# Kernel tuning notes

Hardware: AMD Instinct MI355X
Metric: run time of the kernel (lower is better)

Reference implementation:

```python
import jax, jax.numpy as jnp
import numpy as np

H, W, C = 384, 384, 200
HIDE, CNN_OUT, NCLS = 128, 64, 16
N = H * W
E = 1179648
EPS = 1e-5  # torch BatchNorm eps


def _bn(x, g, b, axes):
    # training-mode batch norm (biased variance), matches torch BN in train mode
    m = x.mean(axes, keepdims=True)
    v = x.var(axes, keepdims=True)
    return (x - m) * jax.lax.rsqrt(v + EPS) * g + b


def _gcn(x, w, bias, src, dst, n):
    # PyG GCNConv: add self loops, symmetric D^-1/2 (A+I) D^-1/2 normalization
    h = x @ w  # [N, out]
    loop = jnp.arange(n, dtype=src.dtype)
    s = jnp.concatenate([src, loop])
    d = jnp.concatenate([dst, loop])
    deg = jax.ops.segment_sum(jnp.ones(s.shape, x.dtype), d, num_segments=n)
    dinv = jnp.where(deg > 0, jax.lax.rsqrt(jnp.maximum(deg, 1.0)) * (deg > 0), 0.0)
    norm = dinv[s] * dinv[d]  # [E+N]
    out = jax.ops.segment_sum(h[s] * norm[:, None], d, num_segments=n)
    return out + bias


def _gnn_layer(x, bn_g, bn_b, w, b, src, dst):
    # F.normalize (row L2) -> BN1d -> GCNConv -> LeakyReLU (dropout off in eval)
    nrm = jnp.linalg.norm(x, axis=1, keepdims=True)
    x = x / jnp.maximum(nrm, 1e-12)
    x = _bn(x, bn_g, bn_b, (0,))
    return jax.nn.leaky_relu(_gcn(x, w, b, src, dst, x.shape[0]))


def setup_inputs() -> dict:
    key = jax.random.key(0)
    ks = jax.random.split(key, 16)
    p = {}
    p["x"] = jax.random.normal(ks[0], (H, W, C), jnp.float32)
    p["edge_index"] = jax.random.randint(ks[1], (2, E), 0, N, jnp.int32)
    # CNN_denoise: BN(C) -> 1x1 conv C->128 -> BN(128) -> 1x1 conv 128->128
    p["dn_bn1_g"] = jnp.ones((C,), jnp.float32); p["dn_bn1_b"] = jnp.zeros((C,), jnp.float32)
    p["dn_w1"] = jax.random.normal(ks[2], (C, HIDE), jnp.float32) * 0.05
    p["dn_b1"] = jnp.zeros((HIDE,), jnp.float32)
    p["dn_bn2_g"] = jnp.ones((HIDE,), jnp.float32); p["dn_bn2_b"] = jnp.zeros((HIDE,), jnp.float32)
    p["dn_w2"] = jax.random.normal(ks[3], (HIDE, HIDE), jnp.float32) * 0.05
    p["dn_b2"] = jnp.zeros((HIDE,), jnp.float32)
    # CNNCONV(128,64,k=5): BN(128) -> point 1x1 128->64 (no bias) -> depthwise 5x5 (bias)
    p["cnn_bn_g"] = jnp.ones((HIDE,), jnp.float32); p["cnn_bn_b"] = jnp.zeros((HIDE,), jnp.float32)
    p["cnn_pw"] = jax.random.normal(ks[4], (HIDE, CNN_OUT), jnp.float32) * 0.05
    p["cnn_dw"] = jax.random.normal(ks[5], (CNN_OUT, 1, 5, 5), jnp.float32) * 0.05
    p["cnn_db"] = jnp.zeros((CNN_OUT,), jnp.float32)
    # GCN branch: GNN(128,128), GNN(128,128), GNN(128,64)
    dims = [(HIDE, HIDE), (HIDE, HIDE), (HIDE, CNN_OUT)]
    for i, (di, do) in enumerate(dims, 1):
        p[f"g{i}_bn_g"] = jnp.ones((di,), jnp.float32)
        p[f"g{i}_bn_b"] = jnp.zeros((di,), jnp.float32)
        p[f"g{i}_w"] = jax.random.normal(ks[5 + i], (di, do), jnp.float32) * 0.05
        p[f"g{i}_b"] = jnp.zeros((do,), jnp.float32)
    p["lin_w"] = jax.random.normal(ks[9], (HIDE, NCLS), jnp.float32) * 0.05
    p["lin_b"] = jnp.zeros((NCLS,), jnp.float32)
    return p


def reference(x, edge_index,
              dn_bn1_g, dn_bn1_b, dn_w1, dn_b1, dn_bn2_g, dn_bn2_b, dn_w2, dn_b2,
              cnn_bn_g, cnn_bn_b, cnn_pw, cnn_dw, cnn_db,
              g1_bn_g, g1_bn_b, g1_w, g1_b,
              g2_bn_g, g2_bn_b, g2_w, g2_b,
              g3_bn_g, g3_bn_b, g3_w, g3_b,
              lin_w, lin_b):
    src, dst = edge_index[0], edge_index[1]
    # CNN_denoise (channel-last; 1x1 convs are matmuls)
    h = _bn(x, dn_bn1_g, dn_bn1_b, (0, 1))
    h = jax.nn.leaky_relu(h @ dn_w1 + dn_b1)
    h = _bn(h, dn_bn2_g, dn_bn2_b, (0, 1))
    clean = jax.nn.leaky_relu(h @ dn_w2 + dn_b2)       # [H,W,128]
    flat = clean.reshape(N, HIDE)
    # CNN branch: BN -> 1x1 -> LeakyReLU -> depthwise 5x5 -> LeakyReLU
    c = _bn(clean, cnn_bn_g, cnn_bn_b, (0, 1))
    c = jax.nn.leaky_relu(c @ cnn_pw)                  # [H,W,64]
    cn = c.transpose(2, 0, 1)[None]                    # [1,64,H,W]
    cn = jax.lax.conv_general_dilated(
        cn, cnn_dw, (1, 1), 'SAME', feature_group_count=CNN_OUT,
        dimension_numbers=('NCHW', 'OIHW', 'NCHW'))
    cn = jax.nn.leaky_relu(cn[0].transpose(1, 2, 0) + cnn_db)
    cnn_res = cn.reshape(N, CNN_OUT)
    # GCN branch (3 layers)
    g = _gnn_layer(flat, g1_bn_g, g1_bn_b, g1_w, g1_b, src, dst)
    g = _gnn_layer(g, g2_bn_g, g2_bn_b, g2_w, g2_b, src, dst)
    g = _gnn_layer(g, g3_bn_g, g3_bn_b, g3_w, g3_b, src, dst)
    y = jnp.concatenate([g, cnn_res], axis=-1) @ lin_w + lin_b
    return jax.nn.softmax(y, axis=-1)
```

## Files before the change

kernel.cpp:

```cpp
#include <hip/hip_runtime.h>
#include <stddef.h>

#define HH 384
#define WW 384
#define CC 200
#define NN 147456
#define EE 1179648
#define HIDE 128
#define COUT 64
#define NCLS 16
#define BN_EPS 1e-5f

#define SREP 16
#define SLOTF (512 * SREP)
#define DBINS 64

#define NBKT 72
#define NPBK 288
#define EPB  4096

using u16 = unsigned short;
typedef __attribute__((ext_vector_type(8))) short short8;
typedef __attribute__((ext_vector_type(4))) float float4v;

__device__ __forceinline__ float b2f(u16 u) {
    union { unsigned int i; float f; } v; v.i = ((unsigned int)u) << 16; return v.f;
}
__device__ __forceinline__ u16 f2b(float f) {
    union { float f; unsigned int i; } v; v.f = f;
    unsigned int x = v.i;
    unsigned int r = (x + 0x7fffu + ((x >> 16) & 1u)) >> 16;
    return (u16)r;
}
__device__ __forceinline__ float lrelu(float v) { return v > 0.f ? v : 0.01f * v; }

__global__ void sniff(const u16* __restrict__ x, int* __restrict__ flag) {
    __shared__ int cntS;
    if (threadIdx.x == 0) cntS = 0;
    __syncthreads();
    int c = 0;
    for (int i = 0; i < 8; i++) {
        u16 h = x[threadIdx.x * 8 + i];
        int hb = (h >> 8) & 0x7F;
        if (hb >= 0x3C && hb <= 0x41) c++;
    }
    atomicAdd(&cntS, c);
    __syncthreads();
    if (threadIdx.x == 0) *flag = (cntS < 1536) ? 1 : 0;
}

#define NPAR 27
struct PConv { const void* src[NPAR]; int n[NPAR]; int off[NPAR]; };

__global__ void convert_params(PConv pc, const int* __restrict__ flag,
                               u16* __restrict__ dst) {
    int b = blockIdx.x;
    int n = pc.n[b];
    const void* s = pc.src[b];
    u16* d = dst + pc.off[b];
    int isf = *flag;
    if (isf) {
        const float* sf = (const float*)s;
        for (int i = threadIdx.x; i < n; i += 256) d[i] = f2b(sf[i]);
    } else {
        const u16* sh = (const u16*)s;
        for (int i = threadIdx.x; i < n; i += 256) d[i] = sh[i];
    }
}

__global__ __launch_bounds__(256) void stats200(const void* __restrict__ X,
                                                const int* __restrict__ flag,
                                                float* __restrict__ arena) {
    __shared__ __align__(16) u16 s[128 * 200];
    int t = threadIdx.x;
    int r0 = blockIdx.x * 128;
    if (*flag) {
        const float* Xf = (const float*)X;
        for (int i = t; i < 128 * 25; i += 256) {
            int r = i / 25, kc = i - r * 25;
            const float* p = Xf + (size_t)(r0 + r) * CC + kc * 8;
            float4v a = *(const float4v*)p;
            float4v b = *(const float4v*)(p + 4);
            short8 v;
            #pragma unroll
            for (int j = 0; j < 4; j++) { v[j] = (short)f2b(a[j]); v[4 + j] = (short)f2b(b[j]); }
            *(short8*)&s[r * 200 + kc * 8] = v;
        }
    } else {
        const u16* Xh = (const u16*)X;
        for (int i = t; i < 128 * 25; i += 256) {
            int r = i / 25, kc = i - r * 25;
            *(short8*)&s[r * 200 + kc * 8] =
                *(const short8*)(Xh + (size_t)(r0 + r) * CC + kc * 8);
        }
    }
    __syncthreads();
    if (t < CC) {
        float sum = 0.f, sq = 0.f;
        for (int r = 0; r < 128; r++) {
            float v = b2f(s[r * 200 + t]);
            sum += v; sq += v * v;
        }
        float* rep = arena + (blockIdx.x & (SREP - 1)) * 512;
        atomicAdd(&rep[t], sum);
        atomicAdd(&rep[256 + t], sq);
    }
}

template<int K, int KPAD, int O>
__global__ __launch_bounds__(256) void fold_bn(
        const float* __restrict__ arena, float invN,
        const u16* __restrict__ bng, const u16* __restrict__ bnb,
        const u16* __restrict__ Wsrc, const u16* __restrict__ extrab,
        u16* __restrict__ WT, float* __restrict__ cb) {
    __shared__ float aS[KPAD], sS[KPAD];
    int t = threadIdx.x;
    if (t < KPAD) {
        float a = 0.f, sh = 0.f;
        if (t < K) {
            float sum = 0.f, sq = 0.f;
            #pragma unroll
            for (int r = 0; r < SREP; r++) {
                sum += arena[r * 512 + t];
                sq  += arena[r * 512 + 256 + t];
            }
            float m = sum * invN;
            float var = fmaxf(sq * invN - m * m, 0.f);
            a = b2f(bng[t]) * rsqrtf(var + BN_EPS);
            sh = b2f(bnb[t]) - m * a;
        }
        aS[t] = a; sS[t] = sh;
    }
    __syncthreads();
    int g = t >> 6, l = t & 63;
    int o = blockIdx.x * 4 + g;
    if (o < O) {
        float c = 0.f;
        #pragma unroll
        for (int k = l; k < KPAD; k += 64) {
            float w = (k < K) ? b2f(Wsrc[k * O + o]) : 0.f;
            c += sS[k] * w;
            WT[o * KPAD + k] = f2b(aS[k] * w);
        }
        #pragma unroll
        for (int s = 32; s >= 1; s >>= 1) c += __shfl_down(c, s);
        if (l == 0) cb[o] = c + (extrab ? b2f(extrab[o]) : 0.f);
    }
}

template<int KT, int KSRC, int O, bool LEAKY, bool SCALE, int STATS, bool DUAL>
__global__ __launch_bounds__(256) void gemm_mfma(
        const void* __restrict__ Ap, const u16* __restrict__ WT,
        const float* __restrict__ cb, const float* __restrict__ s1,
        const float* __restrict__ s2, const int* __restrict__ f32p,
        u16* __restrict__ out, float* __restrict__ stA,
        float* __restrict__ stB, float* __restrict__ invn,
        u16* __restrict__ out2) {
    constexpr int KPAD = KT * 32;
    constexpr int LDA = KPAD + 8;
    constexpr int CHR = KPAD / 8;
    constexpr int CHD = KSRC / 8;
    constexpr int NCT = O / 16;
    constexpr int CPW = NCT / 4;
    __shared__ __align__(16) u16 As[64 * LDA];
    __shared__ float rS[4][64];
    __shared__ float invS[64];
    __shared__ float sS1[64], sS2[64];
    int tid = threadIdx.x;
    int row0 = blockIdx.x * 64;

    int isf = f32p ? *f32p : 0;
    if (isf) {
        const float* A = (const float*)Ap;
        for (int i = tid; i < 64 * CHR; i += 256) {
            int r = i / CHR, kc = i - r * CHR;
            short8 v = {0, 0, 0, 0, 0, 0, 0, 0};
            if (kc < CHD) {
                const float* p = A + (size_t)(row0 + r) * KSRC + kc * 8;
                float4v a = *(const float4v*)p;
                float4v b = *(const float4v*)(p + 4);
                #pragma unroll
                for (int j = 0; j < 4; j++) { v[j] = (short)f2b(a[j]); v[4 + j] = (short)f2b(b[j]); }
            }
            *(short8*)&As[r * LDA + kc * 8] = v;
        }
    } else {
        const u16* A = (const u16*)Ap;
        for (int i = tid; i < 64 * CHR; i += 256) {
            int r = i / CHR, kc = i - r * CHR;
            short8 v = {0, 0, 0, 0, 0, 0, 0, 0};
            if (kc < CHD)
                v = *(const short8*)(A + (size_t)(row0 + r) * KSRC + kc * 8);
            *(short8*)&As[r * LDA + kc * 8] = v;
        }
    }
    if (SCALE && tid < 64) { sS1[tid] = s1[row0 + tid]; sS2[tid] = s2[row0 + tid]; }
    __syncthreads();

    int w = tid >> 6, lane = tid & 63, m = lane & 15, q = lane >> 4;
    float4v acc[4][CPW];
    #pragma unroll
    for (int mf = 0; mf < 4; mf++)
        #pragma unroll
        for (int cp = 0; cp < CPW; cp++)
            acc[mf][cp] = (float4v){0.f, 0.f, 0.f, 0.f};

    const u16* Abp = &As[m * LDA + q * 8];
    const u16* Bbp = WT + (size_t)((w * CPW) * 16 + m) * KPAD + q * 8;

    #pragma unroll
    for (int kt = 0; kt < KT; kt++) {
        short8 af[4];
        #pragma unroll
        for (int mf = 0; mf < 4; mf++)
            af[mf] = *(const short8*)(Abp + mf * 16 * LDA + kt * 32);
        #pragma unroll
        for (int cp = 0; cp < CPW; cp++) {
            short8 bf = *(const short8*)(Bbp + (size_t)cp * 16 * KPAD + kt * 32);
            #pragma unroll
            for (int mf = 0; mf < 4; mf++)
                acc[mf][cp] = __builtin_amdgcn_mfma_f32_16x16x32_bf16(
                    af[mf], bf, acc[mf][cp], 0, 0, 0);
        }
    }

    float rp[4][4] = {};
    #pragma unroll
    for (int cp = 0; cp < CPW; cp++) {
        int ct = w * CPW + cp;
        int col = ct * 16 + m;
        float cbv = cb[col];
        #pragma unroll
        for (int mf = 0; mf < 4; mf++) {
            #pragma unroll
            for (int r = 0; r < 4; r++) {
                int rl = mf * 16 + q * 4 + r;
                float x = acc[mf][cp][r];
                if constexpr (DUAL) {
                    if (ct < 8) {
                        x = (x * sS1[rl] + cbv) * sS2[rl];
                        out[(size_t)(row0 + rl) * 128 + col] = f2b(x);
                    } else {
                        x = lrelu(x + cbv);
                        out2[(size_t)(row0 + rl) * 64 + (col - 128)] = f2b(x);
                    }
                } else {
                    if constexpr (SCALE) x = (x * sS1[rl] + cbv) * sS2[rl];
                    else                 x += cbv;
                    if constexpr (LEAKY) x = lrelu(x);
                    out[(size_t)(row0 + rl) * O + col] = f2b(x);
                }
                acc[mf][cp][r] = x;
                if constexpr (STATS == 2) rp[mf][r] += x * x;
            }
        }
    }

    if constexpr (STATS == 2) {
        #pragma unroll
        for (int mf = 0; mf < 4; mf++) {
            #pragma unroll
            for (int r = 0; r < 4; r++) {
                float v = rp[mf][r];
                v += __shfl_xor(v, 1); v += __shfl_xor(v, 2);
                v += __shfl_xor(v, 4); v += __shfl_xor(v, 8);
                if (m == 0) rS[w][mf * 16 + q * 4 + r] = v;
            }
        }
        __syncthreads();
        if (tid < 64) {
            float ss = rS[0][tid] + rS[1][tid] + rS[2][tid] + rS[3][tid];
            float inv = 1.0f / fmaxf(sqrtf(ss), 1e-12f);
            invS[tid] = inv;
            invn[row0 + tid] = inv;
        }
        __syncthreads();
    }

    if constexpr (STATS >= 1) {
        float* stAr = stA + (blockIdx.x & (SREP - 1)) * 512;
        float* stBr = (STATS == 2) ? stB + (blockIdx.x & (SREP - 1)) * 512 : nullptr;
        #pragma unroll
        for (int cp = 0; cp < CPW; cp++) {
            int col = (w * CPW + cp) * 16 + m;
            float cs = 0.f, cq = 0.f, ns = 0.f, nq = 0.f;
            #pragma unroll
            for (int mf = 0; mf < 4; mf++) {
                #pragma unroll
                for (int r = 0; r < 4; r++) {
                    float x = acc[mf][cp][r];
                    cs += x; cq += x * x;
                    if constexpr (STATS == 2) {
                        float nv = x * invS[mf * 16 + q * 4 + r];
                        ns += nv; nq += nv * nv;
                    }
                }
            }
            cs += __shfl_xor(cs, 16); cs += __shfl_xor(cs, 32);
            cq += __shfl_xor(cq, 16); cq += __shfl_xor(cq, 32);
            if constexpr (STATS == 2) {
                ns += __shfl_xor(ns, 16); ns += __shfl_xor(ns, 32);
                nq += __shfl_xor(nq, 16); nq += __shfl_xor(nq, 32);
            }
            if (q == 0) {
                atomicAdd(&stAr[col], cs);
                atomicAdd(&stAr[256 + col], cq);
                if constexpr (STATS == 2) {
                    atomicAdd(&stBr[col], ns);
                    atomicAdd(&stBr[256 + col], nq);
                }
            }
        }
    }
}

__global__ __launch_bounds__(256) void count_bkt(const int* __restrict__ edst,
                                                 int* __restrict__ counts) {
    __shared__ int h[NBKT];
    int t = threadIdx.x, blk = blockIdx.x;
    if (t < NBKT) h[t] = 0;
    __syncthreads();
    int base = blk * EPB;
    for (int i = t; i < EPB; i += 256) {
        unsigned d = (unsigned)edst[base + i];
        if (d < (unsigned)NN) atomicAdd(&h[d >> 11], 1);
    }
    __syncthreads();
    if (t < NBKT) counts[t * NPBK + blk] = h[t];
}

__global__ void scan_bkt(int* __restrict__ counts, int* __restrict__ bbase) {
    __shared__ int bs[NBKT], bb[NBKT];
    int t = threadIdx.x;
    if (t < NBKT) {
        int s = 0;
        for (int i = 0; i < NPBK; i++) s += counts[t * NPBK + i];
        bs[t] = s;
    }
    __syncthreads();
    if (t == 0) {
        int a = 0;
        for (int b = 0; b < NBKT; b++) { bb[b] = a; bbase[b] = a; a += bs[b]; }
        bbase[NBKT] = a;
    }
    __syncthreads();
    if (t < NBKT) {
        int run = bb[t];
        for (int i = 0; i < NPBK; i++) {
            int c = counts[t * NPBK + i];
            counts[t * NPBK + i] = run;
            run += c;
        }
    }
}

__global__ __launch_bounds__(256) void part_bkt(const int* __restrict__ esrc,
                                                const int* __restrict__ edst,
                                                const int* __restrict__ counts,
                                                int2* __restrict__ bpair) {
    __shared__ int cur[NBKT];
    int t = threadIdx.x, blk = blockIdx.x;
    if (t < NBKT) cur[t] = counts[t * NPBK + blk];
    __syncthreads();
    int base = blk * EPB;
    for (int i = t; i < EPB; i += 256) {
        unsigned d = (unsigned)edst[base + i];
        if (d < (unsigned)NN) {
            int pos = atomicAdd(&cur[d >> 11], 1);
            int2 p; p.x = esrc[base + i]; p.y = (int)d;
            bpair[pos] = p;
        }
    }
}

__global__ __launch_bounds__(256) void csr_build(const int2* __restrict__ bpair,
                                                 const int* __restrict__ bbase,
                                                 int* __restrict__ offv,
                                                 int* __restrict__ csr) {
    __shared__ int cntL[2048];
    __shared__ int exL[2048];
    __shared__ int tsum[256];
    int b = blockIdx.x, t = threadIdx.x;
    int e0 = bbase[b], e1 = bbase[b + 1];
    int n0 = b << 11;
    for (int i = t; i < 2048; i += 256) cntL[i] = 0;
    __syncthreads();
    for (int k = e0 + t; k < e1; k += 256) {
        int2 p = bpair[k];
        atomicAdd(&cntL[p.y & 2047], 1);
    }
    __syncthreads();
    int s = 0;
    #pragma unroll
    for (int j = 0; j < 8; j++) s += cntL[t * 8 + j];
    tsum[t] = s;
    __syncthreads();
    for (int o = 1; o < 256; o <<= 1) {
        int x = (t >= o) ? tsum[t - o] : 0;
        __syncthreads();
        tsum[t] += x;
        __syncthreads();
    }
    int run = tsum[t] - s;
    #pragma unroll
    for (int j = 0; j < 8; j++) { int c = cntL[t * 8 + j]; exL[t * 8 + j] = run; run += c; }
    __syncthreads();
    for (int i = t; i < 2048; i += 256) offv[n0 + i] = e0 + exL[i];
    if (b == NBKT - 1 && t == 0) offv[NN] = e1;
    for (int i = t; i < 2048; i += 256) cntL[i] = 0;
    __syncthreads();
    for (int k = e0 + t; k < e1; k += 256) {
        int2 p = bpair[k];
        int l = p.y & 2047;
        int pos = e0 + exL[l] + atomicAdd(&cntL[l], 1);
        csr[pos] = p.x;
    }
}

__global__ void mkdinv2(const int* __restrict__ offv, float* __restrict__ dinv) {
    int i = blockIdx.x * 256 + threadIdx.x;
    dinv[i] = rsqrtf((float)(offv[i + 1] - offv[i]) + 1.0f);
}

__global__ void deg_hist(const int* __restrict__ offv, int* __restrict__ dbin) {
    __shared__ int h[DBINS];
    int t = threadIdx.x;
    if (t < DBINS) h[t] = 0;
    __syncthreads();
    int i = blockIdx.x * 256 + t;
    int dg = offv[i + 1] - offv[i];
    if (dg < 0) dg = 0; if (dg > DBINS - 1) dg = DBINS - 1;
    atomicAdd(&h[dg], 1);
    __syncthreads();
    if (t < DBINS) atomicAdd(&dbin[t], h[t]);
}
__global__ void deg_scan(const int* __restrict__ dbin, int* __restrict__ dbase) {
    if (threadIdx.x == 0) {
        int a = 0;
        for (int b = DBINS - 1; b >= 0; b--) { dbase[b] = a; a += dbin[b]; }
    }
}
__global__ void deg_scatter(const int* __restrict__ offv, int* __restrict__ dbase,
                            int* __restrict__ perm) {
    __shared__ int h[DBINS], base[DBINS];
    int t = threadIdx.x;
    if (t < DBINS) h[t] = 0;
    __syncthreads();
    int i = blockIdx.x * 256 + t;
    int dg = offv[i + 1] - offv[i];
    if (dg < 0) dg = 0; if (dg > DBINS - 1) dg = DBINS - 1;
    atomicAdd(&h[dg], 1);
    __syncthreads();
    if (t < DBINS) { base[t] = atomicAdd(&dbase[t], h[t]); h[t] = 0; }
    __syncthreads();
    int lp = atomicAdd(&h[dg], 1);
    perm[base[dg] + lp] = i;
}

template<int O, int STATS, int GRP>
__global__ __launch_bounds__(256) void aggregate(
        const u16* __restrict__ h2, const int* __restrict__ offv,
        const int* __restrict__ csr, const float* __restrict__ dinv,
        const u16* __restrict__ gb, u16* __restrict__ outp,
        float* __restrict__ stA, float* __restrict__ invn,
        const int* __restrict__ perm) {
    constexpr int CH = O / 8;
    constexpr int NPB = 256 / CH;
    __shared__ float colS[O], colQ[O];
    int t = threadIdx.x;
    if (STATS && t < O) { colS[t] = 0.f; colQ[t] = 0.f; }
    int local = t / CH, c = t % CH;
    size_t cof = (size_t)c * 8;
    const u16* hb = h2 + cof;
    short8 gv = *(const short8*)(gb + cof);
    float sreg[8] = {0.f, 0.f, 0.f, 0.f, 0.f, 0.f, 0.f, 0.f};
    float qreg[8] = {0.f, 0.f, 0.f, 0.f, 0.f, 0.f, 0.f, 0.f};

    #pragma unroll
    for (int g = 0; g < GRP; g++) {
        int pos = blockIdx.x * (NPB * GRP) + g * NPB + local;
        int d = perm[pos];
        float acc[8];
        short8 selfv = *(const short8*)(hb + (size_t)d * O);
        #pragma unroll
        for (int j = 0; j < 8; j++) acc[j] = b2f((u16)selfv[j]);
        int e0 = offv[d], e1 = offv[d + 1];
        if (e0 < 0) e0 = 0;
        if (e1 > EE) e1 = EE;
        int k = e0;
        for (; k + 8 <= e1; k += 8) {
            unsigned i0 = (unsigned)csr[k],     i1 = (unsigned)csr[k + 1];
            unsigned i2 = (unsigned)csr[k + 2], i3 = (unsigned)csr[k + 3];
            unsigned i4 = (unsigned)csr[k + 4], i5 = (unsigned)csr[k + 5];
            unsigned i6 = (unsigned)csr[k + 6], i7 = (unsigned)csr[k + 7];
            short8 v0 = *(const short8*)(hb + (size_t)i0 * O);
            short8 v1 = *(const short8*)(hb + (size_t)i1 * O);
            short8 v2 = *(const short8*)(hb + (size_t)i2 * O);
            short8 v3 = *(const short8*)(hb + (size_t)i3 * O);
            short8 v4 = *(const short8*)(hb + (size_t)i4 * O);
            short8 v5 = *(const short8*)(hb + (size_t)i5 * O);
            short8 v6 = *(const short8*)(hb + (size_t)i6 * O);
            short8 v7 = *(const short8*)(hb + (size_t)i7 * O);
            #pragma unroll
            for (int j = 0; j < 8; j++)
                acc[j] += ((b2f((u16)v0[j]) + b2f((u16)v1[j])) +
                           (b2f((u16)v2[j]) + b2f((u16)v3[j]))) +
                          ((b2f((u16)v4[j]) + b2f((u16)v5[j])) +
                           (b2f((u16)v6[j]) + b2f((u16)v7[j])));
        }
        if (k + 4 <= e1) {
            unsigned i0 = (unsigned)csr[k],     i1 = (unsigned)csr[k + 1];
            unsigned i2 = (unsigned)csr[k + 2], i3 = (unsigned)csr[k + 3];
            short8 v0 = *(const short8*)(hb + (size_t)i0 * O);
            short8 v1 = *(const short8*)(hb + (size_t)i1 * O);
            short8 v2 = *(const short8*)(hb + (size_t)i2 * O);
            short8 v3 = *(const short8*)(hb + (size_t)i3 * O);
            #pragma unroll
            for (int j = 0; j < 8; j++)
                acc[j] += (b2f((u16)v0[j]) + b2f((u16)v1[j])) +
                          (b2f((u16)v2[j]) + b2f((u16)v3[j]));
            k += 4;
        }
        if (k + 2 <= e1) {
            unsigned i0 = (unsigned)csr[k], i1 = (unsigned)csr[k + 1];
            short8 v0 = *(const short8*)(hb + (size_t)i0 * O);
            short8 v1 = *(const short8*)(hb + (size_t)i1 * O);
            #pragma unroll
            for (int j = 0; j < 8; j++)
                acc[j] += b2f((u16)v0[j]) + b2f((u16)v1[j]);
            k += 2;
        }
        if (k < e1) {
            unsigned i0 = (unsigned)csr[k];
            short8 v0 = *(const short8*)(hb + (size_t)i0 * O);
            #pragma unroll
            for (int j = 0; j < 8; j++) acc[j] += b2f((u16)v0[j]);
        }
        float dd = dinv[d];
        float outv[8];
        short8 res;
        #pragma unroll
        for (int j = 0; j < 8; j++) {
            outv[j] = lrelu(dd * acc[j] + b2f((u16)gv[j]));
            res[j] = (short)f2b(outv[j]);
        }
        *(short8*)(outp + (size_t)d * O + cof) = res;

        if constexpr (STATS) {
            float ss = 0.f;
            #pragma unroll
            for (int j = 0; j < 8; j++) ss += outv[j] * outv[j];
            ss += __shfl_xor(ss, 1); ss += __shfl_xor(ss, 2);
            ss += __shfl_xor(ss, 4); ss += __shfl_xor(ss, 8);
            float inv = 1.0f / fmaxf(sqrtf(ss), 1e-12f);
            if (c == 0) invn[d] = inv;
            #pragma unroll
            for (int j = 0; j < 8; j++) {
                float nv = outv[j] * inv;
                sreg[j] += nv; qreg[j] += nv * nv;
            }
        }
    }

    if constexpr (STATS) {
        __syncthreads();
        #pragma unroll
        for (int j = 0; j < 8; j++) {
            float s = sreg[j];
            s += __shfl_xor(s, 16); s += __shfl_xor(s, 32);
            float qq = qreg[j];
            qq += __shfl_xor(qq, 16); qq += __shfl_xor(qq, 32);
            if ((t & 63) < 16) {
                atomicAdd(&colS[c * 8 + j], s);
                atomicAdd(&colQ[c * 8 + j], qq);
            }
        }
        __syncthreads();
        if (t < O) {
            float* rep = stA + (blockIdx.x & (SREP - 1)) * 512;
            atomicAdd(&rep[t], colS[t]);
            atomicAdd(&rep[256 + t], colQ[t]);
        }
    }
}

__global__ __launch_bounds__(256) void final_fused(
        const u16* __restrict__ g3, const u16* __restrict__ cpre,
        const u16* __restrict__ dwW, const u16* __restrict__ db,
        const u16* __restrict__ lw, const u16* __restrict__ lb,
        const int* __restrict__ flag, void* __restrict__ outp) {
    __shared__ __align__(16) u16 tile[400 * 72];
    __shared__ __align__(16) u16 wT[25 * 64];
    __shared__ __align__(16) u16 wL[2048];
    __shared__ float bDW[64];
    __shared__ float bL[16];
    int t = threadIdx.x;
    int tx = blockIdx.x % 24, ty = blockIdx.x / 24;
    int x0 = tx * 16 - 2, y0 = ty * 16 - 2;
    for (int i = t; i < 1600; i += 256) {
        int f = i / 25, tap = i - f * 25;
        wT[tap * 64 + f] = dwW[i];
    }
    for (int i = t; i < 2048; i += 256) wL[i] = lw[i];
    if (t < 64) bDW[t] = b2f(db[t]);
    if (t < 16) bL[t] = b2f(lb[t]);
    for (int u = t; u < 3200; u += 256) {
        int pix = u >> 3, c8 = u & 7;
        int gy = y0 + pix / 20, gx = x0 + pix % 20;
        short8 v = {0, 0, 0, 0, 0, 0, 0, 0};
        if (gy >= 0 && gy < HH && gx >= 0 && gx < WW)
            v = *(const short8*)(cpre + ((size_t)(gy * WW + gx)) * 64 + c8 * 8);
        *(short8*)&tile[pix * 72 + c8 * 8] = v;
    }
    __syncthreads();

    int px = t & 15, py = t >> 4;
    int node = (ty * 16 + py) * WW + tx * 16 + px;
    float y[16];
    #pragma unroll
    for (int o = 0; o < 16; o++) y[o] = bL[o];

    const u16* g3p = g3 + (size_t)node * 64;
    for (int c8 = 0; c8 < 8; c8++) {
        short8 gvv = *(const short8*)(g3p + c8 * 8);
        #pragma unroll
        for (int j = 0; j < 8; j++) {
            float g = b2f((u16)gvv[j]);
            const short8 w0 = *(const short8*)&wL[(c8 * 8 + j) * 16];
            const short8 w1 = *(const short8*)&wL[(c8 * 8 + j) * 16 + 8];
            #pragma unroll
            for (int o = 0; o < 8; o++) {
                y[o]     += g * b2f((u16)w0[o]);
                y[o + 8] += g * b2f((u16)w1[o]);
            }
        }
    }
    for (int c8 = 0; c8 < 8; c8++) {
        float acc[8] = {0.f, 0.f, 0.f, 0.f, 0.f, 0.f, 0.f, 0.f};
        #pragma unroll
        for (int dy = 0; dy < 5; dy++) {
            int rbase = ((py + dy) * 20 + px) * 72 + c8 * 8;
            #pragma unroll
            for (int dx = 0; dx < 5; dx++) {
                short8 v  = *(const short8*)&tile[rbase + dx * 72];
                short8 wv = *(const short8*)&wT[(dy * 5 + dx) * 64 + c8 * 8];
                #pragma unroll
                for (int j = 0; j < 8; j++)
                    acc[j] += b2f((u16)v[j]) * b2f((u16)wv[j]);
            }
        }
        #pragma unroll
        for (int j = 0; j < 8; j++) {
            float cv = lrelu(acc[j] + bDW[c8 * 8 + j]);
            int f = 64 + c8 * 8 + j;
            const short8 w0 = *(const short8*)&wL[f * 16];
            const short8 w1 = *(const short8*)&wL[f * 16 + 8];
            #pragma unroll
            for (int o = 0; o < 8; o++) {
                y[o]     += cv * b2f((u16)w0[o]);
                y[o + 8] += cv * b2f((u16)w1[o]);
            }
        }
    }
    float mx = y[0];
    #pragma unroll
    for (int o = 1; o < 16; o++) mx = fmaxf(mx, y[o]);
    float sum = 0.f;
    #pragma unroll
    for (int o = 0; o < 16; o++) { y[o] = __expf(y[o] - mx); sum += y[o]; }
    float inv = 1.0f / fmaxf(sum, 1e-30f);
    if (*flag) {
        float* of = (float*)outp;
        #pragma unroll
        for (int o = 0; o < 16; o++) of[(size_t)node * 16 + o] = y[o] * inv;
    } else {
        u16* oh = (u16*)outp;
        #pragma unroll
        for (int o = 0; o < 16; o++) oh[(size_t)node * 16 + o] = f2b(y[o] * inv);
    }
}

extern "C" void kernel_launch(void* const* d_in, const int* in_sizes, int n_in,
                              void* d_out, int out_size, void* d_ws, size_t ws_size,
                              hipStream_t stream) {
    const void* X   = d_in[0];
    const int* EIDX = (const int*)d_in[1];
    const int* esrc = EIDX;
    const int* edst = EIDX + EE;

    char* ws = (char*)d_ws;
    size_t off = 0;
    auto alloc = [&](size_t sz) -> char* {
        size_t szr = (sz + 255) & ~(size_t)255;
        char* p;
        if (off + szr <= ws_size) { p = ws + off; off += szr; }
        else { p = ws; }
        return p;
    };

    int*   dflag   = (int*)alloc(256);
    static const int pidx[NPAR] = {2,3,4,5,6,7,8,9,10,11,12,13,14,
                                   15,16,17,18,19,20,21,22,23,24,25,26,27,28};
    static const int pn[NPAR]   = {200,200,25600,128,128,128,16384,128,
                                   128,128,8192,1600,64,
                                   128,128,16384,128,
                                   128,128,16384,128,
                                   128,128,8192,64,
                                   2048,16};
    u16* parena = (u16*)alloc(100352 * 2);
    PConv pc;
    {
        int po = 0;
        for (int i = 0; i < NPAR; i++) {
            pc.src[i] = d_in[pidx[i]];
            pc.n[i] = pn[i];
            pc.off[i] = po;
            po += (pn[i] + 15) & ~15;
        }
    }
    const u16* DN1G = parena + pc.off[0];
    const u16* DN1B = parena + pc.off[1];
    const u16* DNW1 = parena + pc.off[2];
    const u16* DNB1 = parena + pc.off[3];
    const u16* DN2G = parena + pc.off[4];
    const u16* DN2B = parena + pc.off[5];
    const u16* DNW2 = parena + pc.off[6];
    const u16* DNB2 = parena + pc.off[7];
    const u16* CBNG = parena + pc.off[8];
    const u16* CBNB = parena + pc.off[9];
    const u16* CPW  = parena + pc.off[10];
    const u16* CDW  = parena + pc.off[11];
    const u16* CDB  = parena + pc.off[12];
    const u16* G1G  = parena + pc.off[13];
    const u16* G1B  = parena + pc.off[14];
    const u16* G1W  = parena + pc.off[15];
    const u16* G1BI = parena + pc.off[16];
    const u16* G2G  = parena + pc.off[17];
    const u16* G2B  = parena + pc.off[18];
    const u16* G2W  = parena + pc.off[19];
    const u16* G2BI = parena + pc.off[20];
    const u16* G3G  = parena + pc.off[21];
    const u16* G3B  = parena + pc.off[22];
    const u16* G3W  = parena + pc.off[23];
    const u16* G3BI = parena + pc.off[24];
    const u16* LINW = parena + pc.off[25];
    const u16* LINB = parena + pc.off[26];

    float* arena   = (float*)alloc((size_t)6 * SLOTF * 4);
    int*   dbin    = (int*)alloc(DBINS * 4);
    int*   counts  = (int*)alloc((size_t)NBKT * NPBK * 4);
    int*   bbase   = (int*)alloc((NBKT + 1) * 4);
    int2*  bpair   = (int2*)alloc((size_t)EE * 8);
    int*   offv    = (int*)alloc((size_t)(NN + 1) * 4);
    int*   dbase   = (int*)alloc(DBINS * 4);
    int*   perm    = (int*)alloc((size_t)NN * 4);
    float* dinvp   = (float*)alloc((size_t)NN * 4);
    float* invnorm = (float*)alloc((size_t)NN * 4);
    u16*   W1T     = (u16*)alloc(128 * 224 * 2);
    u16*   W2T     = (u16*)alloc(128 * 128 * 2);
    u16*   WgT     = (u16*)alloc(192 * 128 * 2);
    float* cb1     = (float*)alloc(128 * 4);
    float* cb2     = (float*)alloc(128 * 4);
    float* cbg     = (float*)alloc(192 * 4);
    int*   csr     = (int*)alloc((size_t)EE * 4);
    u16*   cbuf    = (u16*)alloc((size_t)NN * 64 * 2);
    u16*   big1    = (u16*)alloc((size_t)NN * 128 * 2);
    u16*   big2    = (u16*)alloc((size_t)NN * 128 * 2);

    const float invN = 1.0f / (float)NN;
    size_t zsz = (size_t)((char*)dbin + 256 - (char*)arena);
    size_t zcap = ((char*)arena >= ws && (size_t)((char*)arena - ws) < ws_size)
                      ? ws_size - (size_t)((char*)arena - ws) : 0;
    if (zsz > zcap) zsz = zcap;
    hipMemsetAsync(arena, 0, zsz, stream);

    sniff<<<1, 256, 0, stream>>>((const u16*)X, dflag);
    convert_params<<<NPAR, 256, 0, stream>>>(pc, dflag, parena);

    count_bkt<<<NPBK, 256, 0, stream>>>(edst, counts);
    scan_bkt<<<1, 128, 0, stream>>>(counts, bbase);
    part_bkt<<<NPBK, 256, 0, stream>>>(esrc, edst, counts, bpair);
    csr_build<<<NBKT, 256, 0, stream>>>(bpair, bbase, offv, csr);
    mkdinv2<<<NN / 256, 256, 0, stream>>>(offv, dinvp);
    deg_hist<<<NN / 256, 256, 0, stream>>>(offv, dbin);
    deg_scan<<<1, 64, 0, stream>>>(dbin, dbase);
    deg_scatter<<<NN / 256, 256, 0, stream>>>(offv, dbase, perm);

    stats200<<<1152, 256, 0, stream>>>(X, dflag, arena + 0 * SLOTF);
    fold_bn<200, 224, 128><<<32, 256, 0, stream>>>(arena + 0 * SLOTF, invN, DN1G, DN1B, DNW1, DNB1, W1T, cb1);
    gemm_mfma<7, 200, 128, true, false, 1, false><<<NN / 64, 256, 0, stream>>>(
        X, W1T, cb1, nullptr, nullptr, dflag, big1, arena + 1 * SLOTF, nullptr, nullptr, nullptr);
    fold_bn<128, 128, 128><<<32, 256, 0, stream>>>(arena + 1 * SLOTF, invN, DN2G, DN2B, DNW2, DNB2, W2T, cb2);
    gemm_mfma<4, 128, 128, true, false, 2, false><<<NN / 64, 256, 0, stream>>>(
        big1, W2T, cb2, nullptr, nullptr, nullptr, big2, arena + 2 * SLOTF, arena + 3 * SLOTF, invnorm, nullptr);

    fold_bn<128, 128, 128><<<32, 256, 0, stream>>>(arena + 3 * SLOTF, invN, G1G, G1B, G1W, nullptr, WgT, cbg);
    fold_bn<128, 128, 64><<<16, 256, 0, stream>>>(arena + 2 * SLOTF, invN, CBNG, CBNB, CPW, nullptr,
                                                  WgT + 128 * 128, cbg + 128);
    gemm_mfma<4, 128, 192, false, true, 0, true><<<NN / 64, 256, 0, stream>>>(
        big2, WgT, cbg, invnorm, dinvp, nullptr, big1, nullptr, nullptr, nullptr, cbuf);
    aggregate<128, 1, 4><<<NN / 64, 256, 0, stream>>>(
        big1, offv, csr, dinvp, G1BI, big2, arena + 4 * SLOTF, invnorm, perm);

    fold_bn<128, 128, 128><<<32, 256, 0, stream>>>(arena + 4 * SLOTF, invN, G2G, G2B, G2W, nullptr, WgT, cbg);
    gemm_mfma<4, 128, 128, false, true, 0, false><<<NN / 64, 256, 0, stream>>>(
        big2, WgT, cbg, invnorm, dinvp, nullptr, big1, nullptr, nullptr, nullptr, nullptr);
    aggregate<128, 1, 4><<<NN / 64, 256, 0, stream>>>(
        big1, offv, csr, dinvp, G2BI, big2, arena + 5 * SLOTF, invnorm, perm);

    fold_bn<128, 128, 64><<<16, 256, 0, stream>>>(arena + 5 * SLOTF, invN, G3G, G3B, G3W, nullptr, WgT, cbg);
    gemm_mfma<4, 128, 64, false, true, 0, false><<<NN / 64, 256, 0, stream>>>(
        big2, WgT, cbg, invnorm, dinvp, nullptr, big1, nullptr, nullptr, nullptr, nullptr);
    aggregate<64, 0, 1><<<NN / 32, 256, 0, stream>>>(
        big1, offv, csr, dinvp, G3BI, big2, nullptr, nullptr, perm);

    final_fused<<<576, 256, 0, stream>>>(big2, cbuf, CDW, CDB, LINW, LINB, dflag, d_out);

    (void)in_sizes; (void)n_in; (void)out_size;
}
```

Measured before the change: 760.1 us.

## Use direct global-to-LDS loads with XOR swizzle, stage partition writes, fuse degree kernels

The GEMM A-tile staging now uses global_load_lds to copy bf16 rows straight into shared memory. It replaces the padded row stride with an XOR-swizzled layout to avoid bank conflicts, and points a zero-filled buffer at padding chunks. The edge partition kernel first buckets edges locally in shared memory and then writes them out contiguously per bucket, which avoids scattered global writes. The dinv and degree-histogram kernels are merged into one. The risks are higher LDS use in the partition kernel and the correctness of the swizzle index mapping for the K=200 case.

```diff
diff --git a/kernel.cpp b/kernel.cpp
--- a/kernel.cpp
+++ b/kernel.cpp
@@ -33,6 +33,12 @@
     return (u16)r;
 }
 __device__ __forceinline__ float lrelu(float v) { return v > 0.f ? v : 0.01f * v; }
+
+__device__ __forceinline__ void gload_lds16(const void* g, void* l) {
+    __builtin_amdgcn_global_load_lds(
+        (const __attribute__((address_space(1))) void*)g,
+        (__attribute__((address_space(3))) void*)l, 16, 0, 0);
+}
 
 __global__ void sniff(const u16* __restrict__ x, int* __restrict__ flag) {
     __shared__ int cntS;
@@ -155,14 +161,17 @@
         const float* __restrict__ s2, const int* __restrict__ f32p,
         u16* __restrict__ out, float* __restrict__ stA,
         float* __restrict__ stB, float* __restrict__ invn,
-        u16* __restrict__ out2) {
+        u16* __restrict__ out2, const u16* __restrict__ zpad) {
     constexpr int KPAD = KT * 32;
-    constexpr int LDA = KPAD + 8;
-    constexpr int CHR = KPAD / 8;
     constexpr int CHD = KSRC / 8;
+    constexpr int ROWCH = ((KT * 4 + 7) / 8) * 8;
+    constexpr int ROWE = ROWCH * 8;
+    constexpr int LPR = ROWCH;
+    constexpr int RPI = 64 / LPR;
+    constexpr int NSI = 64 / RPI;
     constexpr int NCT = O / 16;
     constexpr int CPW = NCT / 4;
-    __shared__ __align__(16) u16 As[64 * LDA];
+    __shared__ __align__(16) u16 As[64 * ROWE];
     __shared__ float rS[4][64];
     __shared__ float invS[64];
     __shared__ float sS1[64], sS2[64];
@@ -172,26 +181,31 @@
     int isf = f32p ? *f32p : 0;
     if (isf) {
         const float* A = (const float*)Ap;
-        for (int i = tid; i < 64 * CHR; i += 256) {
-            int r = i / CHR, kc = i - r * CHR;
+        for (int i = tid; i < 64 * ROWCH; i += 256) {
+            int r = i / ROWCH, slot = i - r * ROWCH;
+            int chunk = slot ^ (r & 7);
             short8 v = {0, 0, 0, 0, 0, 0, 0, 0};
-            if (kc < CHD) {
-                const float* p = A + (size_t)(row0 + r) * KSRC + kc * 8;
+            if (chunk < CHD) {
+                const float* p = A + (size_t)(row0 + r) * KSRC + chunk * 8;
                 float4v a = *(const float4v*)p;
                 float4v b = *(const float4v*)(p + 4);
                 #pragma unroll
                 for (int j = 0; j < 4; j++) { v[j] = (short)f2b(a[j]); v[4 + j] = (short)f2b(b[j]); }
             }
-            *(short8*)&As[r * LDA + kc * 8] = v;
+            *(short8*)&As[r * ROWE + slot * 8] = v;
         }
     } else {
         const u16* A = (const u16*)Ap;
-        for (int i = tid; i < 64 * CHR; i += 256) {
-            int r = i / CHR, kc = i - r * CHR;
-            short8 v = {0, 0, 0, 0, 0, 0, 0, 0};
-            if (kc < CHD)
-                v = *(const short8*)(A + (size_t)(row0 + r) * KSRC + kc * 8);
-            *(short8*)&As[r * LDA + kc * 8] = v;
+        int l = tid & 63, wv = tid >> 6;
+        int rl0 = l / LPR, cL = l - rl0 * LPR;
+        #pragma unroll
+        for (int s = 0; s < NSI / 4; s++) {
+            int si = wv + s * 4;
+            int rL = si * RPI + rl0;
+            int chunk = cL ^ (rL & 7);
+            const u16* src = (chunk < CHD)
+                ? A + (size_t)(row0 + rL) * KSRC + chunk * 8 : zpad;
+            gload_lds16(src, (char*)As + si * 1024);
         }
     }
     if (SCALE && tid < 64) { sS1[tid] = s1[row0 + tid]; sS2[tid] = s2[row0 + tid]; }
@@ -205,15 +219,15 @@
         for (int cp = 0; cp < CPW; cp++)
             acc[mf][cp] = (float4v){0.f, 0.f, 0.f, 0.f};
 
-    const u16* Abp = &As[m * LDA + q * 8];
     const u16* Bbp = WT + (size_t)((w * CPW) * 16 + m) * KPAD + q * 8;
 
     #pragma unroll
     for (int kt = 0; kt < KT; kt++) {
         short8 af[4];
+        int slot = (kt * 4 + q) ^ (m & 7);
         #pragma unroll
         for (int mf = 0; mf < 4; mf++)
-            af[mf] = *(const short8*)(Abp + mf * 16 * LDA + kt * 32);
+            af[mf] = *(const short8*)&As[(size_t)(mf * 16 + m) * ROWE + slot * 8];
         #pragma unroll
         for (int cp = 0; cp < CPW; cp++) {
             short8 bf = *(const short8*)(Bbp + (size_t)cp * 16 * KPAD + kt * 32);
@@ -358,18 +372,44 @@
                                                 const int* __restrict__ edst,
                                                 const int* __restrict__ counts,
                                                 int2* __restrict__ bpair) {
-    __shared__ int cur[NBKT];
+    __shared__ int2 buf[EPB];
+    __shared__ int lcnt[NBKT], lbase[NBKT], gbase[NBKT];
     int t = threadIdx.x, blk = blockIdx.x;
-    if (t < NBKT) cur[t] = counts[t * NPBK + blk];
+    if (t < NBKT) lcnt[t] = 0;
     __syncthreads();
     int base = blk * EPB;
-    for (int i = t; i < EPB; i += 256) {
-        unsigned d = (unsigned)edst[base + i];
-        if (d < (unsigned)NN) {
-            int pos = atomicAdd(&cur[d >> 11], 1);
-            int2 p; p.x = esrc[base + i]; p.y = (int)d;
-            bpair[pos] = p;
-        }
+    int dv[16], sv[16];
+    #pragma unroll
+    for (int j = 0; j < 16; j++) {
+        dv[j] = edst[base + t + j * 256];
+        sv[j] = esrc[base + t + j * 256];
+        unsigned ud = (unsigned)dv[j];
+        if (ud < (unsigned)NN) atomicAdd(&lcnt[ud >> 11], 1);
+    }
+    __syncthreads();
+    if (t == 0) {
+        int a = 0;
+        for (int b = 0; b < NBKT; b++) { lbase[b] = a; a += lcnt[b]; }
+    }
+    __syncthreads();
+    if (t < NBKT) { gbase[t] = counts[t * NPBK + blk]; lcnt[t] = 0; }
+    __syncthreads();
+    #pragma unroll
+    for (int j = 0; j < 16; j++) {
+        unsigned ud = (unsigned)dv[j];
+        if (ud < (unsigned)NN) {
+            int b = ud >> 11;
+            int p = lbase[b] + atomicAdd(&lcnt[b], 1);
+            int2 e; e.x = sv[j]; e.y = (int)ud;
+            buf[p] = e;
+        }
+    }
+    __syncthreads();
+    int tot = lbase[NBKT - 1] + lcnt[NBKT - 1];
+    for (int i = t; i < tot; i += 256) {
+        int2 p = buf[i];
+        int b = ((unsigned)p.y) >> 11;
+        bpair[gbase[b] + (i - lbase[b])] = p;
     }
 }
 
@@ -417,20 +457,18 @@
     }
 }
 
-__global__ void mkdinv2(const int* __restrict__ offv, float* __restrict__ dinv) {
-    int i = blockIdx.x * 256 + threadIdx.x;
-    dinv[i] = rsqrtf((float)(offv[i + 1] - offv[i]) + 1.0f);
-}
-
-__global__ void deg_hist(const int* __restrict__ offv, int* __restrict__ dbin) {
+__global__ void mkdinv_deghist(const int* __restrict__ offv,
+                               float* __restrict__ dinv, int* __restrict__ dbin) {
     __shared__ int h[DBINS];
     int t = threadIdx.x;
     if (t < DBINS) h[t] = 0;
     __syncthreads();
     int i = blockIdx.x * 256 + t;
     int dg = offv[i + 1] - offv[i];
-    if (dg < 0) dg = 0; if (dg > DBINS - 1) dg = DBINS - 1;
-    atomicAdd(&h[dg], 1);
+    if (dg < 0) dg = 0;
+    dinv[i] = rsqrtf((float)dg + 1.0f);
+    int dc = dg > DBINS - 1 ? DBINS - 1 : dg;
+    atomicAdd(&h[dc], 1);
     __syncthreads();
     if (t < DBINS) atomicAdd(&dbin[t], h[t]);
 }
@@ -748,6 +786,7 @@
 
     float* arena   = (float*)alloc((size_t)6 * SLOTF * 4);
     int*   dbin    = (int*)alloc(DBINS * 4);
+    u16*   zpad    = (u16*)alloc(256);
     int*   counts  = (int*)alloc((size_t)NBKT * NPBK * 4);
     int*   bbase   = (int*)alloc((NBKT + 1) * 4);
     int2*  bpair   = (int2*)alloc((size_t)EE * 8);
@@ -768,7 +807,7 @@
     u16*   big2    = (u16*)alloc((size_t)NN * 128 * 2);
 
     const float invN = 1.0f / (float)NN;
-    size_t zsz = (size_t)((char*)dbin + 256 - (char*)arena);
+    size_t zsz = (size_t)((char*)zpad + 256 - (char*)arena);
     size_t zcap = ((char*)arena >= ws && (size_t)((char*)arena - ws) < ws_size)
                       ? ws_size - (size_t)((char*)arena - ws) : 0;
     if (zsz > zcap) zsz = zcap;
@@ -781,36 +820,35 @@
     scan_bkt<<<1, 128, 0, stream>>>(counts, bbase);
     part_bkt<<<NPBK, 256, 0, stream>>>(esrc, edst, counts, bpair);
     csr_build<<<NBKT, 256, 0, stream>>>(bpair, bbase, offv, csr);
-    mkdinv2<<<NN / 256, 256, 0, stream>>>(offv, dinvp);
-    deg_hist<<<NN / 256, 256, 0, stream>>>(offv, dbin);
+    mkdinv_deghist<<<NN / 256, 256, 0, stream>>>(offv, dinvp, dbin);
     deg_scan<<<1, 64, 0, stream>>>(dbin, dbase);
     deg_scatter<<<NN / 256, 256, 0, stream>>>(offv, dbase, perm);
 
     stats200<<<1152, 256, 0, stream>>>(X, dflag, arena + 0 * SLOTF);
     fold_bn<200, 224, 128><<<32, 256, 0, stream>>>(arena + 0 * SLOTF, invN, DN1G, DN1B, DNW1, DNB1, W1T, cb1);
     gemm_mfma<7, 200, 128, true, false, 1, false><<<NN / 64, 256, 0, stream>>>(
-        X, W1T, cb1, nullptr, nullptr, dflag, big1, arena + 1 * SLOTF, nullptr, nullptr, nullptr);
+        X, W1T, cb1, nullptr, nullptr, dflag, big1, arena + 1 * SLOTF, nullptr, nullptr, nullptr, zpad);
     fold_bn<128, 128, 128><<<32, 256, 0, stream>>>(arena + 1 * SLOTF, invN, DN2G, DN2B, DNW2, DNB2, W2T, cb2);
     gemm_mfma<4, 128, 128, true, false, 2, false><<<NN / 64, 256, 0, stream>>>(
-        big1, W2T, cb2, nullptr, nullptr, nullptr, big2, arena + 2 * SLOTF, arena + 3 * SLOTF, invnorm, nullptr);
+        big1, W2T, cb2, nullptr, nullptr, nullptr, big2, arena + 2 * SLOTF, arena + 3 * SLOTF, invnorm, nullptr, zpad);
 
     fold_bn<128, 128, 128><<<32, 256, 0, stream>>>(arena + 3 * SLOTF, invN, G1G, G1B, G1W, nullptr, WgT, cbg);
     fold_bn<128, 128, 64><<<16, 256, 0, stream>>>(arena + 2 * SLOTF, invN, CBNG, CBNB, CPW, nullptr,
                                                   WgT + 128 * 128, cbg + 128);
     gemm_mfma<4, 128, 192, false, true, 0, true><<<NN / 64, 256, 0, stream>>>(
-        big2, WgT, cbg, invnorm, dinvp, nullptr, big1, nullptr, nullptr, nullptr, cbuf);
+        big2, WgT, cbg, invnorm, dinvp, nullptr, big1, nullptr, nullptr, nullptr, cbuf, zpad);
     aggregate<128, 1, 4><<<NN / 64, 256, 0, stream>>>(
         big1, offv, csr, dinvp, G1BI, big2, arena + 4 * SLOTF, invnorm, perm);
 
     fold_bn<128, 128, 128><<<32, 256, 0, stream>>>(arena + 4 * SLOTF, invN, G2G, G2B, G2W, nullptr, WgT, cbg);
     gemm_mfma<4, 128, 128, false, true, 0, false><<<NN / 64, 256, 0, stream>>>(
-        big2, WgT, cbg, invnorm, dinvp, nullptr, big1, nullptr, nullptr, nullptr, nullptr);
+        big2, WgT, cbg, invnorm, dinvp, nullptr, big1, nullptr, nullptr, nullptr, nullptr, zpad);
     aggregate<128, 1, 4><<<NN / 64, 256, 0, stream>>>(
         big1, offv, csr, dinvp, G2BI, big2, arena + 5 * SLOTF, invnorm, perm);
 
     fold_bn<128, 128, 64><<<16, 256, 0, stream>>>(arena + 5 * SLOTF, invN, G3G, G3B, G3W, nullptr, WgT, cbg);
     gemm_mfma<4, 128, 64, false, true, 0, false><<<NN / 64, 256, 0, stream>>>(
-        big2, WgT, cbg, invnorm, dinvp, nullptr, big1, nullptr, nullptr, nullptr, nullptr);
+        big2, WgT, cbg, invnorm, dinvp, nullptr, big1, nullptr, nullptr, nullptr, nullptr, zpad);
     aggregate<64, 0, 1><<<NN / 32, 256, 0, stream>>>(
         big1, offv, csr, dinvp, G3BI, big2, nullptr, nullptr, perm);
 
```

Measured after the change: 745.8 us. No clear change (-1.9%).
